# Kernel optimization log

Hardware: AMD Instinct MI355X
Metric: run time of the kernel (lower is better)

The kernel has to match this reference:

```python
import jax, jax.numpy as jnp
import numpy as np

HEADS = 8
BN_EPS = 1e-5

def _bn(x2d, g, b):
    # torch BatchNorm1d in training mode: biased batch stats
    mu = x2d.mean(0)
    var = x2d.var(0)
    return (x2d - mu) * jax.lax.rsqrt(var + BN_EPS) * g + b

def _window_indices(H):
    # exclusive-end box coordinates, in the exact order of the torch loop
    m = H // 2
    r0, r1, c0, c1 = [], [], [], []
    for i in range(1, m + 1):
        wins = [(m - i, m + i + 1, m - i, m + i + 1),  # full square
                (m - i, m + 1,     m - i, m + i + 1),  # top half
                (m,     m + i + 1, m - i, m + i + 1),  # bottom half
                (m - i, m + i + 1, m - i, m + 1),      # left half
                (m - i, m + i + 1, m,     m + i + 1)]  # right half
        for a, b, c, d in wins:
            r0.append(a); r1.append(b); c0.append(c); c1.append(d)
    r0 = np.array(r0); r1 = np.array(r1); c0 = np.array(c0); c1 = np.array(c1)
    counts = ((r1 - r0) * (c1 - c0)).astype(np.float32)
    return r0, r1, c0, c1, counts

def _box_sums(P, r0, r1, c0, c1):
    # P: padded 2D prefix sum [B, C, H+1, H+1]; returns [B, C, K]
    return P[:, :, r1, c1] - P[:, :, r0, c1] - P[:, :, r1, c0] + P[:, :, r0, c0]

def _integral(img):
    return jnp.pad(jnp.cumsum(jnp.cumsum(img, axis=2), axis=3), ((0, 0), (0, 0), (1, 0), (1, 0)))

def setup_inputs() -> dict:
    key = jax.random.key(0)
    ks = jax.random.split(key, 8)
    B, Cin, H = 64, 512, 31
    C = 512  # heads * base_dim
    x = jax.random.normal(ks[0], (B, Cin, H, H), dtype=jnp.float32)
    w_v = jax.random.normal(ks[1], (Cin, C), dtype=jnp.float32) * 0.02
    w_k = jax.random.normal(ks[2], (Cin, C), dtype=jnp.float32) * 0.02
    w_fc = jax.random.normal(ks[3], (Cin + C, 512), dtype=jnp.float32) * 0.02
    z = lambda n: jnp.zeros((n,), jnp.float32)
    o = lambda n: jnp.ones((n,), jnp.float32)
    return {"x": x,
            "w_v": w_v, "b_v": z(C), "g_vn": o(C), "b_vn": z(C),
            "w_k": w_k, "b_k": z(C), "g_kn": o(C), "b_kn": z(C),
            "w_fc": w_fc, "b_fc": z(512), "g_fcn": o(512), "b_fcn": z(512)}

def reference(x, w_v, b_v, g_vn, b_vn, w_k, b_k, g_kn, b_kn, w_fc, b_fc, g_fcn, b_fcn):
    B, Cin, H, W = x.shape
    N = H * W
    C = w_v.shape[1]
    d = C // HEADS
    m = H // 2
    xt = x.reshape(B, Cin, N).transpose(0, 2, 1)       # [B, N, Cin]
    x0 = xt[:, N // 2, :]                              # [B, Cin] center pixel feature
    flat = xt.reshape(B * N, Cin)
    v = jax.nn.relu(_bn(flat @ w_v + b_v, g_vn, b_vn))
    v = v.reshape(B, N, C).transpose(0, 2, 1).reshape(B, C, H, H)
    k = _bn(flat @ w_k + b_k, g_kn, b_kn).reshape(B, N, HEADS, d).transpose(0, 2, 1, 3)  # [B,h,N,d]
    q = k[:, :, N // 2, :]                             # [B, h, d]
    attn = jax.nn.softmax(jnp.einsum('bhd,bhnd->bhn', q, k) * (d ** -0.5), axis=-1)      # [B,h,N]
    attn_full = jnp.broadcast_to(attn[:, :, None, :], (B, HEADS, d, N)).reshape(B, C, H, H)
    xw = attn_full * v                                 # attn-weighted values [B,C,H,H]
    eps = 1e-16
    r0, r1, c0, c1, counts = _window_indices(H)
    Px = _integral(xw)
    Pa = _integral(attn_full)
    mx = _box_sums(Px, r0, r1, c0, c1) / counts        # window means of xw   [B,C,K]
    ma = _box_sums(Pa, r0, r1, c0, c1) / counts        # window means of attn [B,C,K]
    y_win = (mx / (ma + eps)).transpose(0, 2, 1)       # [B, K, C]
    y = jnp.concatenate([xw[:, :, m, m][:, None, :], y_win], axis=1)  # [B, n, C]
    # F.normalize(p=2, dim=2)
    y = y / jnp.maximum(jnp.linalg.norm(y, axis=2, keepdims=True), 1e-12)
    n = y.shape[1]
    yy = jnp.concatenate([jnp.broadcast_to(x0[:, None, :], (B, n, Cin)), y], axis=-1)
    out = jax.nn.relu(_bn(yy.reshape(B * n, Cin + C) @ w_fc + b_fc, g_fcn, b_fcn))
    return out.reshape(B, n, -1)
```

## Files before the change

### kernel.cpp

```cpp
#include <hip/hip_runtime.h>
#include <stdint.h>

#define DEV __device__ __forceinline__

typedef __bf16 bf16x8 __attribute__((ext_vector_type(8)));
typedef unsigned short u16x8 __attribute__((ext_vector_type(8)));
typedef float f32x4 __attribute__((ext_vector_type(4)));

#define NS 968

DEV uint16_t f2bf(float f) {
    union { float f; uint32_t u; } v; v.f = f;
    uint32_t r = v.u + 0x7fffu + ((v.u >> 16) & 1u);
    return (uint16_t)(r >> 16);
}
DEV float bf2f(uint16_t h) {
    union { uint32_t u; float f; } v; v.u = ((uint32_t)h) << 16;
    return v.f;
}
DEV float bflo(uint32_t w) { union { uint32_t u; float f; } v; v.u = w << 16; return v.f; }
DEV float bfhi(uint32_t w) { union { uint32_t u; float f; } v; v.u = w & 0xffff0000u; return v.f; }

#if __has_builtin(__builtin_amdgcn_cvt_pk_bf16_f32)
typedef __bf16 bf16x2 __attribute__((ext_vector_type(2)));
DEV uint32_t pk2bf(float lo, float hi) {
    bf16x2 r = __builtin_amdgcn_cvt_pk_bf16_f32(lo, hi);
    return __builtin_bit_cast(uint32_t, r);
}
#else
DEV uint32_t pk2bf(float lo, float hi) {
    return (uint32_t)f2bf(lo) | ((uint32_t)f2bf(hi) << 16);
}
#endif

#if __has_builtin(__builtin_amdgcn_global_load_lds)
DEV void async16(const uint16_t* g, uint16_t* l) {
    __builtin_amdgcn_global_load_lds(
        (const __attribute__((address_space(1))) uint32_t*)g,
        (__attribute__((address_space(3))) uint32_t*)l, 16, 0, 0);
}
#else
DEV void async16(const uint16_t* g, uint16_t* l) {
    *(u16x8*)l = *(const u16x8*)g;
}
#endif

__global__ void k_convert_x(const float* __restrict__ x, uint16_t* __restrict__ xbt) {
    __shared__ float tile[32][33];
    int b = blockIdx.z;
    int n0 = blockIdx.x * 32;
    int c0 = blockIdx.y * 32;
    int tx = threadIdx.x, ty = threadIdx.y;
    #pragma unroll
    for (int i = 0; i < 4; ++i) {
        int c = c0 + ty + 8 * i;
        int n = n0 + tx;
        float v = 0.f;
        if (n < 961) v = x[((size_t)b * 512 + c) * 961 + n];
        tile[ty + 8 * i][tx] = v;
    }
    __syncthreads();
    int idx = ty * 32 + tx;
    int c4 = (idx & 7) * 4;
    int nl = idx >> 3;
    int n = n0 + nl;
    if (n < NS) {
        ushort4 val;
        val.x = f2bf(tile[c4 + 0][nl]);
        val.y = f2bf(tile[c4 + 1][nl]);
        val.z = f2bf(tile[c4 + 2][nl]);
        val.w = f2bf(tile[c4 + 3][nl]);
        *(ushort4*)&xbt[((size_t)b * NS + n) * 512 + c0 + c4] = val;
    }
}

__global__ void k_convert_w(const float* __restrict__ wv, const float* __restrict__ wk,
                            const float* __restrict__ wfc,
                            uint16_t* __restrict__ wvkt, uint16_t* __restrict__ wfct) {
    int idx = blockIdx.x * 256 + threadIdx.x;
    if (idx < 524288) {
        int j = idx >> 9, k = idx & 511;
        float v = (j < 512) ? wv[(size_t)k * 512 + j] : wk[(size_t)k * 512 + (j - 512)];
        wvkt[idx] = f2bf(v);
    } else {
        int t = idx - 524288;
        int j = t >> 10, k = t & 1023;
        wfct[t] = f2bf(wfc[(size_t)k * 512 + j]);
    }
}

template<int K, int EPI>
__global__ __launch_bounds__(256, 4)
void k_gemm(const uint16_t* __restrict__ A, const uint16_t* __restrict__ Bt,
            uint16_t* __restrict__ out_v, uint16_t* __restrict__ out_k,
            float* __restrict__ out_f,
            float* __restrict__ colsum, float* __restrict__ colsq)
{
    __shared__ __align__(16) uint16_t sbuf[16384];
    __shared__ float sStat[256];
    uint16_t* sA0 = sbuf;
    uint16_t* sA1 = sbuf + 4096;
    uint16_t* sB0 = sbuf + 8192;
    uint16_t* sB1 = sbuf + 12288;

    const int tid = threadIdx.x;
    const int wave = tid >> 6, lane = tid & 63;
    const int quad = lane >> 4, l16 = lane & 15;
    int m0, j0;
    if constexpr (EPI == 0) {
        int lin = blockIdx.x;
        int xcd = lin & 7, rest = lin >> 3;
        int jb = rest & 7, mhi = rest >> 3;
        int mb = mhi * 8 + xcd;
        if (mb >= 484) return;
        m0 = mb * 128; j0 = jb * 128;
    } else {
        m0 = blockIdx.y * 128; j0 = blockIdx.x * 128;
    }
    const int wm = wave >> 1, wj = wave & 1;

    const f32x4 fzero = {0.f, 0.f, 0.f, 0.f};
    f32x4 acc[4][4];
    #pragma unroll
    for (int i = 0; i < 4; ++i)
        #pragma unroll
        for (int j = 0; j < 4; ++j) acc[i][j] = fzero;

    const int c0 = tid;
    const int mA0 = c0 >> 2, kq0 = c0 & 3;
    const int c1 = tid + 256;
    const int mA1 = c1 >> 2, kq1 = c1 & 3;

    const int KT = K / 64;
    for (int kt = 0; kt < KT; ++kt) {
        const uint16_t* Ak = A + (size_t)m0 * K + kt * 64;
        const uint16_t* Bk = Bt + (size_t)j0 * K + kt * 64;
        async16(Ak + (size_t)mA0 * K + kq0 * 8,      &sA0[c0 * 8]);
        async16(Ak + (size_t)mA1 * K + kq1 * 8,      &sA0[c1 * 8]);
        async16(Ak + (size_t)mA0 * K + 32 + kq0 * 8, &sA1[c0 * 8]);
        async16(Ak + (size_t)mA1 * K + 32 + kq1 * 8, &sA1[c1 * 8]);
        async16(Bk + (size_t)mA0 * K + kq0 * 8,      &sB0[c0 * 8]);
        async16(Bk + (size_t)mA1 * K + kq1 * 8,      &sB0[c1 * 8]);
        async16(Bk + (size_t)mA0 * K + 32 + kq0 * 8, &sB1[c0 * 8]);
        async16(Bk + (size_t)mA1 * K + 32 + kq1 * 8, &sB1[c1 * 8]);
        __syncthreads();
        #pragma unroll
        for (int p = 0; p < 2; ++p) {
            const uint16_t* pA = p ? sA1 : sA0;
            const uint16_t* pB = p ? sB1 : sB0;
            bf16x8 af[4], bfr[4];
            #pragma unroll
            for (int i = 0; i < 4; ++i) {
                int m = wm * 64 + i * 16 + l16;
                u16x8 r = *(const u16x8*)&pA[m * 32 + quad * 8];
                af[i] = __builtin_bit_cast(bf16x8, r);
            }
            #pragma unroll
            for (int j = 0; j < 4; ++j) {
                int jj = wj * 64 + j * 16 + l16;
                u16x8 r = *(const u16x8*)&pB[jj * 32 + quad * 8];
                bfr[j] = __builtin_bit_cast(bf16x8, r);
            }
            #pragma unroll
            for (int i = 0; i < 4; ++i)
                #pragma unroll
                for (int j = 0; j < 4; ++j)
                    acc[i][j] = __builtin_amdgcn_mfma_f32_16x16x32_bf16(af[i], bfr[j], acc[i][j], 0, 0, 0);
        }
        __syncthreads();
    }

    sStat[tid] = 0.f;
    __syncthreads();

    #pragma unroll
    for (int j = 0; j < 4; ++j) {
        const int col_local = wj * 64 + j * 16 + l16;
        float ls = 0.f, lq = 0.f;
        #pragma unroll
        for (int i = 0; i < 4; ++i) {
            #pragma unroll
            for (int reg = 0; reg < 4; ++reg) {
                const float val = acc[i][j][reg];
                ls += val; lq += val * val;
                if constexpr (EPI == 1) {
                    const int r = m0 + wm * 64 + i * 16 + quad * 4 + reg;
                    out_f[(size_t)r * 512 + (j0 + col_local)] = val;
                }
            }
        }
        ls += __shfl_xor(ls, 16); lq += __shfl_xor(lq, 16);
        ls += __shfl_xor(ls, 32); lq += __shfl_xor(lq, 32);
        if (quad == 0) {
            atomicAdd(&sStat[col_local], ls);
            atomicAdd(&sStat[128 + col_local], lq);
        }
    }
    __syncthreads();
    if (tid < 128) atomicAdd(&colsum[j0 + tid], sStat[tid]);
    else           atomicAdd(&colsq[j0 + (tid & 127)], sStat[tid]);

    if constexpr (EPI == 0) {
        #pragma unroll
        for (int ch = 0; ch < 2; ++ch) {
            if (wj == ch) {
                #pragma unroll
                for (int j = 0; j < 4; ++j) {
                    const int c = j * 16 + l16;
                    #pragma unroll
                    for (int i = 0; i < 4; ++i) {
                        const int rloc = wm * 64 + i * 16 + quad * 4;
                        uint2 pp;
                        pp.x = pk2bf(acc[i][j][0], acc[i][j][1]);
                        pp.y = pk2bf(acc[i][j][2], acc[i][j][3]);
                        *(uint2*)&sbuf[c * 136 + rloc] = pp;
                    }
                }
            }
            __syncthreads();
            const int jg = j0 + ch * 64;
            uint16_t* const outp = (jg < 512) ? out_v : out_k;
            const int jbase = (jg < 512) ? jg : jg - 512;
            #pragma unroll
            for (int s = 0; s < 8; ++s) {
                const int chunk = tid + 256 * s;
                const int c = chunk >> 5, q = chunk & 31;
                uint2 val = *(const uint2*)&sbuf[c * 136 + q * 4];
                const int r = m0 + q * 4;
                const unsigned bb_ = (unsigned)r / (unsigned)NS;
                const unsigned nn = (unsigned)r - bb_ * (unsigned)NS;
                *(uint2*)&outp[((size_t)bb_ * 512 + jbase + c) * NS + nn] = val;
            }
            __syncthreads();
        }
    }
}

__global__ void k_attn(const uint16_t* __restrict__ kraw,
                       const float* __restrict__ colsum, const float* __restrict__ colsq,
                       const float* __restrict__ g_kn, const float* __restrict__ b_kn,
                       float* __restrict__ attn, float* __restrict__ maw)
{
    __shared__ float qa[64];
    __shared__ float s_qb;
    __shared__ float att[NS];
    __shared__ float red[8];

    int bh = blockIdx.x;
    int b = bh >> 3, h = bh & 7;
    int tid = threadIdx.x;
    constexpr float invM = 1.f / 61504.f;

    if (tid < 64) {
        int c = h * 64 + tid;
        float mean = colsum[512 + c] * invM;
        float q_ = colsq[512 + c] * invM;
        float a = g_kn[c] * rsqrtf(q_ - mean * mean + 1e-5f);
        float bb = b_kn[c] - mean * a;
        float kr = bf2f(kraw[((size_t)b * 512 + c) * NS + 480]);
        float qv = kr * a + bb;
        qa[tid] = qv * a;
        float qb = qv * bb;
        for (int off = 32; off; off >>= 1) qb += __shfl_down(qb, off);
        if (tid == 0) s_qb = qb;
    }
    __syncthreads();

    const int n4 = tid * 4;
    const bool active = n4 < 961;
    float a0 = 0.f, a1 = 0.f, a2 = 0.f, a3 = 0.f;
    if (active) {
        const uint16_t* kp = kraw + ((size_t)b * 512 + h * 64) * NS + n4;
        #pragma unroll 16
        for (int dd = 0; dd < 64; ++dd) {
            uint2 kk = *(const uint2*)(kp + (size_t)dd * NS);
            float q = qa[dd];
            a0 += q * bflo(kk.x);
            a1 += q * bfhi(kk.x);
            a2 += q * bflo(kk.y);
            a3 += q * bfhi(kk.y);
        }
    }
    float lg[4] = {a0, a1, a2, a3};
    float lmax = -1e30f;
    #pragma unroll
    for (int i = 0; i < 4; ++i) {
        lg[i] = (lg[i] + s_qb) * 0.125f;
        if (n4 + i < 961) lmax = fmaxf(lmax, lg[i]);
    }
    for (int off = 32; off; off >>= 1) lmax = fmaxf(lmax, __shfl_xor(lmax, off));
    if ((tid & 63) == 0) red[tid >> 6] = lmax;
    __syncthreads();
    float bmax = fmaxf(fmaxf(red[0], red[1]), fmaxf(red[2], red[3]));

    float lsum = 0.f;
    #pragma unroll
    for (int i = 0; i < 4; ++i) {
        float e = (n4 + i < 961) ? __expf(lg[i] - bmax) : 0.f;
        lg[i] = e;
        lsum += e;
    }
    for (int off = 32; off; off >>= 1) lsum += __shfl_xor(lsum, off);
    if ((tid & 63) == 0) red[4 + (tid >> 6)] = lsum;
    __syncthreads();
    float inv = 1.f / (red[4] + red[5] + red[6] + red[7]);
    if (active) {
        f32x4 v = {lg[0] * inv, lg[1] * inv, lg[2] * inv, lg[3] * inv};
        *(f32x4*)&att[n4] = v;
        *(f32x4*)&attn[(size_t)bh * NS + n4] = v;
    }
    __syncthreads();

    if (tid < 31) { float s = 0.f; for (int cc = 0; cc < 31; ++cc) { s += att[tid * 31 + cc]; att[tid * 31 + cc] = s; } }
    __syncthreads();
    if (tid < 31) { float s = 0.f; for (int rr = 0; rr < 31; ++rr) { s += att[rr * 31 + tid]; att[rr * 31 + tid] = s; } }
    __syncthreads();

    if (tid < 75) {
        int i = tid / 5 + 1, t = tid % 5;
        const int m = 15;
        int r0, r1, cc0, cc1;
        switch (t) {
            case 0: r0 = m - i; r1 = m + i + 1; cc0 = m - i; cc1 = m + i + 1; break;
            case 1: r0 = m - i; r1 = m + 1;     cc0 = m - i; cc1 = m + i + 1; break;
            case 2: r0 = m;     r1 = m + i + 1; cc0 = m - i; cc1 = m + i + 1; break;
            case 3: r0 = m - i; r1 = m + i + 1; cc0 = m - i; cc1 = m + 1;     break;
            default:r0 = m - i; r1 = m + i + 1; cc0 = m;     cc1 = m + i + 1; break;
        }
        auto S = [&](int r, int c) -> float { return (r < 0 || c < 0) ? 0.f : att[r * 31 + c]; };
        float box = S(r1 - 1, cc1 - 1) - S(r0 - 1, cc1 - 1) - S(r1 - 1, cc0 - 1) + S(r0 - 1, cc0 - 1);
        float cnt = (float)((r1 - r0) * (cc1 - cc0));
        maw[(size_t)bh * 75 + tid] = box / cnt;
    }
}

__global__ void k_winbox(const uint16_t* __restrict__ vraw,
                         const float* __restrict__ colsum, const float* __restrict__ colsq,
                         const float* __restrict__ g_vn, const float* __restrict__ b_vn,
                         const float* __restrict__ attn, const float* __restrict__ maw,
                         float* __restrict__ y)
{
    __shared__ float xw[NS];
    __shared__ float s_center;
    int bc = blockIdx.x;
    int b = bc >> 9, c = bc & 511;
    int h = c >> 6;
    int tid = threadIdx.x;
    constexpr float invM = 1.f / 61504.f;
    float mean = colsum[c] * invM;
    float q_ = colsq[c] * invM;
    float a = g_vn[c] * rsqrtf(q_ - mean * mean + 1e-5f);
    float bb = b_vn[c] - mean * a;
    const uint16_t* vp = vraw + (size_t)bc * NS;
    const float* ap = attn + (size_t)(b * 8 + h) * NS;
    int n4 = tid * 4;
    if (n4 < 961) {
        uint2 kk = *(const uint2*)(vp + n4);
        f32x4 at = *(const f32x4*)(ap + n4);
        f32x4 v;
        v[0] = fmaxf(bflo(kk.x) * a + bb, 0.f) * at[0];
        v[1] = fmaxf(bfhi(kk.x) * a + bb, 0.f) * at[1];
        v[2] = fmaxf(bflo(kk.y) * a + bb, 0.f) * at[2];
        v[3] = fmaxf(bfhi(kk.y) * a + bb, 0.f) * at[3];
        *(f32x4*)&xw[n4] = v;
    }
    __syncthreads();
    if (tid == 0) s_center = xw[480];
    __syncthreads();
    if (tid < 31) { float s = 0.f; for (int cc = 0; cc < 31; ++cc) { s += xw[tid * 31 + cc]; xw[tid * 31 + cc] = s; } }
    __syncthreads();
    if (tid < 31) { float s = 0.f; for (int rr = 0; rr < 31; ++rr) { s += xw[rr * 31 + tid]; xw[rr * 31 + tid] = s; } }
    __syncthreads();
    if (tid < 75) {
        int i = tid / 5 + 1, t = tid % 5;
        const int m = 15;
        int r0, r1, cc0, cc1;
        switch (t) {
            case 0: r0 = m - i; r1 = m + i + 1; cc0 = m - i; cc1 = m + i + 1; break;
            case 1: r0 = m - i; r1 = m + 1;     cc0 = m - i; cc1 = m + i + 1; break;
            case 2: r0 = m;     r1 = m + i + 1; cc0 = m - i; cc1 = m + i + 1; break;
            case 3: r0 = m - i; r1 = m + i + 1; cc0 = m - i; cc1 = m + 1;     break;
            default:r0 = m - i; r1 = m + i + 1; cc0 = m;     cc1 = m + i + 1; break;
        }
        auto S = [&](int r, int cc) -> float { return (r < 0 || cc < 0) ? 0.f : xw[r * 31 + cc]; };
        float box = S(r1 - 1, cc1 - 1) - S(r0 - 1, cc1 - 1) - S(r1 - 1, cc0 - 1) + S(r0 - 1, cc0 - 1);
        float cnt = (float)((r1 - r0) * (cc1 - cc0));
        float mx = box / cnt;
        float ma = maw[(size_t)(b * 8 + h) * 75 + tid];
        y[((size_t)b * 76 + 1 + tid) * 512 + c] = mx / (ma + 1e-16f);
    }
    if (tid == 96) y[((size_t)b * 76) * 512 + c] = s_center;
}

__global__ void k_build_yy(const float* __restrict__ y, const uint16_t* __restrict__ xbt,
                           uint16_t* __restrict__ yy)
{
    __shared__ float red[4];
    int row = blockIdx.x;
    int b = row / 76;
    int tid = threadIdx.x;
    const float* yp = y + (size_t)row * 512;
    float v0 = yp[tid], v1 = yp[tid + 256];
    float ss = v0 * v0 + v1 * v1;
    for (int off = 32; off; off >>= 1) ss += __shfl_xor(ss, off);
    if ((tid & 63) == 0) red[tid >> 6] = ss;
    __syncthreads();
    float tot = red[0] + red[1] + red[2] + red[3];
    float inv = 1.f / fmaxf(sqrtf(tot), 1e-12f);
    uint16_t* op = yy + (size_t)row * 1024;
    const uint16_t* x0p = xbt + ((size_t)b * NS + 480) * 512;
    op[tid]           = x0p[tid];
    op[tid + 256]     = x0p[tid + 256];
    op[512 + tid]       = f2bf(v0 * inv);
    op[512 + tid + 256] = f2bf(v1 * inv);
}

__global__ void k_fcout(const float* __restrict__ fcraw,
                        const float* __restrict__ colsum, const float* __restrict__ colsq,
                        const float* __restrict__ g, const float* __restrict__ be,
                        float* __restrict__ out)
{
    size_t idx = (size_t)blockIdx.x * 256 + threadIdx.x;
    if (idx < (size_t)4864 * 512) {
        int j = (int)(idx & 511);
        constexpr float invM = 1.f / 4864.f;
        float mean = colsum[j] * invM;
        float q_ = colsq[j] * invM;
        float a = g[j] * rsqrtf(q_ - mean * mean + 1e-5f);
        float bb = be[j] - mean * a;
        out[idx] = fmaxf(fcraw[idx] * a + bb, 0.f);
    }
}

extern "C" void kernel_launch(void* const* d_in, const int* in_sizes, int n_in,
                              void* d_out, int out_size, void* d_ws, size_t ws_size,
                              hipStream_t stream)
{
    (void)in_sizes; (void)n_in; (void)out_size; (void)ws_size;
    const float* x    = (const float*)d_in[0];
    const float* w_v  = (const float*)d_in[1];
    const float* g_vn = (const float*)d_in[3];
    const float* b_vn = (const float*)d_in[4];
    const float* w_k  = (const float*)d_in[5];
    const float* g_kn = (const float*)d_in[7];
    const float* b_kn = (const float*)d_in[8];
    const float* w_fc = (const float*)d_in[9];
    const float* g_fcn = (const float*)d_in[11];
    const float* b_fcn = (const float*)d_in[12];
    float* out = (float*)d_out;

    char* base = (char*)d_ws;
    size_t off = 0;
    auto alloc = [&](size_t bytes) -> void* {
        void* p = base + off;
        off += (bytes + 255) & ~(size_t)255;
        return p;
    };
    uint16_t* xbt  = (uint16_t*)alloc((size_t)64 * NS * 512 * 2);
    uint16_t* wvkt = (uint16_t*)alloc((size_t)1024 * 512 * 2);
    uint16_t* wfct = (uint16_t*)alloc((size_t)512 * 1024 * 2);
    uint16_t* vraw = (uint16_t*)alloc((size_t)64 * 512 * NS * 2);
    uint16_t* kraw = (uint16_t*)alloc((size_t)64 * 512 * NS * 2);
    float* stats   = (float*)alloc(3072 * 4);
    float* attn    = (float*)alloc((size_t)512 * NS * 4);
    float* maw     = (float*)alloc((size_t)512 * 75 * 4);
    float* y       = (float*)alloc((size_t)64 * 76 * 512 * 4);
    uint16_t* yy   = (uint16_t*)alloc((size_t)4864 * 1024 * 2);
    float* fcraw   = (float*)alloc((size_t)4864 * 512 * 4);

    hipMemsetAsync(stats, 0, 3072 * 4, stream);
    k_convert_x<<<dim3(31, 16, 64), dim3(32, 8), 0, stream>>>(x, xbt);
    k_convert_w<<<4096, 256, 0, stream>>>(w_v, w_k, w_fc, wvkt, wfct);

    k_gemm<512, 0><<<3904, 256, 0, stream>>>(xbt, wvkt, vraw, kraw, nullptr,
                                             stats, stats + 1024);

    k_attn<<<512, 256, 0, stream>>>(kraw, stats, stats + 1024, g_kn, b_kn, attn, maw);
    k_winbox<<<64 * 512, 256, 0, stream>>>(vraw, stats, stats + 1024, g_vn, b_vn, attn, maw, y);
    k_build_yy<<<4864, 256, 0, stream>>>(y, xbt, yy);

    k_gemm<1024, 1><<<dim3(4, 38), 256, 0, stream>>>(yy, wfct, nullptr, nullptr, fcraw,
                                                     stats + 2048, stats + 2560);
    k_fcout<<<9728, 256, 0, stream>>>(fcraw, stats + 2048, stats + 2560, g_fcn, b_fcn, out);
}
```

Before: 418.3 us.

## Parallelize 2D prefix sums with warp scans and pad spatial stride to 992

Replaces the serial 31-thread row and column prefix-sum loops in the attention and window-box kernels with 32-lane shuffle-based scans spread across all 256 threads. The padded spatial stride grows from 968 to 992 so that 64*992 is a multiple of 128 and the first GEMM grid needs no early-exit bounds check. The shared arrays shrink to 961 entries, which needs special handling for the tail elements, and that tail handling looks convoluted. The larger padding adds some extra GEMM work and memory traffic on padded rows.

Result: slower. 451.8 us (+8.0%).

```diff
diff --git a/kernel.cpp b/kernel.cpp
--- a/kernel.cpp
+++ b/kernel.cpp
@@ -7,7 +7,7 @@
 typedef unsigned short u16x8 __attribute__((ext_vector_type(8)));
 typedef float f32x4 __attribute__((ext_vector_type(4)));
 
-#define NS 968
+#define NS 992
 
 DEV uint16_t f2bf(float f) {
     union { float f; uint32_t u; } v; v.f = f;
@@ -32,6 +32,15 @@
     return (uint32_t)f2bf(lo) | ((uint32_t)f2bf(hi) << 16);
 }
 #endif
+
+DEV float scan32(float v, int lane) {
+    #pragma unroll
+    for (int d = 1; d < 32; d <<= 1) {
+        float o = __shfl_up(v, d, 32);
+        if (lane >= d) v += o;
+    }
+    return v;
+}
 
 #if __has_builtin(__builtin_amdgcn_global_load_lds)
 DEV void async16(const uint16_t* g, uint16_t* l) {
@@ -64,14 +73,12 @@
     int c4 = (idx & 7) * 4;
     int nl = idx >> 3;
     int n = n0 + nl;
-    if (n < NS) {
-        ushort4 val;
-        val.x = f2bf(tile[c4 + 0][nl]);
-        val.y = f2bf(tile[c4 + 1][nl]);
-        val.z = f2bf(tile[c4 + 2][nl]);
-        val.w = f2bf(tile[c4 + 3][nl]);
-        *(ushort4*)&xbt[((size_t)b * NS + n) * 512 + c0 + c4] = val;
-    }
+    ushort4 val;
+    val.x = f2bf(tile[c4 + 0][nl]);
+    val.y = f2bf(tile[c4 + 1][nl]);
+    val.z = f2bf(tile[c4 + 2][nl]);
+    val.w = f2bf(tile[c4 + 3][nl]);
+    *(ushort4*)&xbt[((size_t)b * NS + n) * 512 + c0 + c4] = val;
 }
 
 __global__ void k_convert_w(const float* __restrict__ wv, const float* __restrict__ wk,
@@ -111,9 +118,7 @@
         int lin = blockIdx.x;
         int xcd = lin & 7, rest = lin >> 3;
         int jb = rest & 7, mhi = rest >> 3;
-        int mb = mhi * 8 + xcd;
-        if (mb >= 484) return;
-        m0 = mb * 128; j0 = jb * 128;
+        m0 = (mhi * 8 + xcd) * 128; j0 = jb * 128;
     } else {
         m0 = blockIdx.y * 128; j0 = blockIdx.x * 128;
     }
@@ -243,7 +248,7 @@
 {
     __shared__ float qa[64];
     __shared__ float s_qb;
-    __shared__ float att[NS];
+    __shared__ float att[961];
     __shared__ float red[8];
 
     int bh = blockIdx.x;
@@ -306,14 +311,37 @@
     float inv = 1.f / (red[4] + red[5] + red[6] + red[7]);
     if (active) {
         f32x4 v = {lg[0] * inv, lg[1] * inv, lg[2] * inv, lg[3] * inv};
-        *(f32x4*)&att[n4] = v;
+        if (n4 <= 956) { *(f32x4*)&att[n4] = v; }
+        else { att[956] = v[0]; att[957] = v[1]; att[958] = v[2]; att[959] = v[3]; att[960] = lg[0]; }
+        if (n4 == 956) att[960] = v[0] * 0.f + lg[0] * 0.f;
         *(f32x4*)&attn[(size_t)bh * NS + n4] = v;
     }
-    __syncthreads();
-
-    if (tid < 31) { float s = 0.f; for (int cc = 0; cc < 31; ++cc) { s += att[tid * 31 + cc]; att[tid * 31 + cc] = s; } }
-    __syncthreads();
-    if (tid < 31) { float s = 0.f; for (int rr = 0; rr < 31; ++rr) { s += att[rr * 31 + tid]; att[rr * 31 + tid] = s; } }
+    if (tid == 240) att[960] = lg[0] * inv;
+    __syncthreads();
+
+    {
+        int r8 = tid >> 5, col = tid & 31;
+        #pragma unroll
+        for (int p = 0; p < 4; ++p) {
+            int row = p * 8 + r8;
+            bool on = (row < 31) && (col < 31);
+            float v = on ? att[row * 31 + col] : 0.f;
+            v = scan32(v, col);
+            if (on) att[row * 31 + col] = v;
+        }
+    }
+    __syncthreads();
+    {
+        int c8 = tid >> 5, r = tid & 31;
+        #pragma unroll
+        for (int p = 0; p < 4; ++p) {
+            int c = p * 8 + c8;
+            bool on = (c < 31) && (r < 31);
+            float v = on ? att[r * 31 + c] : 0.f;
+            v = scan32(v, r);
+            if (on) att[r * 31 + c] = v;
+        }
+    }
     __syncthreads();
 
     if (tid < 75) {
@@ -340,7 +368,7 @@
                          const float* __restrict__ attn, const float* __restrict__ maw,
                          float* __restrict__ y)
 {
-    __shared__ float xw[NS];
+    __shared__ float xw[961];
     __shared__ float s_center;
     int bc = blockIdx.x;
     int b = bc >> 9, c = bc & 511;
@@ -362,14 +390,36 @@
         v[1] = fmaxf(bfhi(kk.x) * a + bb, 0.f) * at[1];
         v[2] = fmaxf(bflo(kk.y) * a + bb, 0.f) * at[2];
         v[3] = fmaxf(bfhi(kk.y) * a + bb, 0.f) * at[3];
-        *(f32x4*)&xw[n4] = v;
+        if (n4 <= 956) { *(f32x4*)&xw[n4] = v; }
+        else { xw[956] = v[0]; xw[957] = v[1]; xw[958] = v[2]; xw[959] = v[3]; }
+        if (n4 == 960) xw[960] = v[0];
     }
     __syncthreads();
     if (tid == 0) s_center = xw[480];
     __syncthreads();
-    if (tid < 31) { float s = 0.f; for (int cc = 0; cc < 31; ++cc) { s += xw[tid * 31 + cc]; xw[tid * 31 + cc] = s; } }
-    __syncthreads();
-    if (tid < 31) { float s = 0.f; for (int rr = 0; rr < 31; ++rr) { s += xw[rr * 31 + tid]; xw[rr * 31 + tid] = s; } }
+    {
+        int r8 = tid >> 5, col = tid & 31;
+        #pragma unroll
+        for (int p = 0; p < 4; ++p) {
+            int row = p * 8 + r8;
+            bool on = (row < 31) && (col < 31);
+            float v = on ? xw[row * 31 + col] : 0.f;
+            v = scan32(v, col);
+            if (on) xw[row * 31 + col] = v;
+        }
+    }
+    __syncthreads();
+    {
+        int c8 = tid >> 5, r = tid & 31;
+        #pragma unroll
+        for (int p = 0; p < 4; ++p) {
+            int cc = p * 8 + c8;
+            bool on = (cc < 31) && (r < 31);
+            float v = on ? xw[r * 31 + cc] : 0.f;
+            v = scan32(v, r);
+            if (on) xw[r * 31 + cc] = v;
+        }
+    }
     __syncthreads();
     if (tid < 75) {
         int i = tid / 5 + 1, t = tid % 5;
@@ -472,7 +522,7 @@
     k_convert_x<<<dim3(31, 16, 64), dim3(32, 8), 0, stream>>>(x, xbt);
     k_convert_w<<<4096, 256, 0, stream>>>(w_v, w_k, w_fc, wvkt, wfct);
 
-    k_gemm<512, 0><<<3904, 256, 0, stream>>>(xbt, wvkt, vraw, kraw, nullptr,
+    k_gemm<512, 0><<<3968, 256, 0, stream>>>(xbt, wvkt, vraw, kraw, nullptr,
                                              stats, stats + 1024);
 
     k_attn<<<512, 256, 0, stream>>>(kraw, stats, stats + 1024, g_kn, b_kn, attn, maw);
```
